# Optimization experiments

Hardware: AMD Instinct MI355X
Metric: run time of the kernel (lower is better)

The kernel has to match this reference:

```python
import jax, jax.numpy as jnp
import numpy as np

N_NODES = 100000
N_EDGES = 1600000
D_IN = 64
D_OUT = 64


def setup_inputs() -> dict:
    key = jax.random.key(0)
    k1, k2, k3, k4, k5 = jax.random.split(key, 5)
    features = jax.random.normal(k1, (N_NODES, D_IN), dtype=jnp.float32)
    edge_rows = jax.random.randint(k2, (N_EDGES,), 0, N_NODES, dtype=jnp.int32)
    edge_cols = jax.random.randint(k3, (N_EDGES,), 0, N_NODES, dtype=jnp.int32)
    edge_vals = jax.random.uniform(k4, (N_EDGES,), dtype=jnp.float32)
    # glorot_uniform init for the dense projection weight
    limit = np.sqrt(6.0 / (D_IN + D_OUT)).astype(np.float32)
    weight = jax.random.uniform(k5, (D_IN, D_OUT), dtype=jnp.float32,
                                minval=-limit, maxval=limit)
    return {"features": features, "edge_rows": edge_rows,
            "edge_cols": edge_cols, "edge_vals": edge_vals, "weight": weight}


def reference(features, edge_rows, edge_cols, edge_vals, weight):
    # SpMM: (adj @ features) via edge-list gather + segment_sum
    gathered = features[edge_cols] * edge_vals[:, None]        # [E, D_IN]
    agg = jax.ops.segment_sum(gathered, edge_rows,
                              num_segments=N_NODES)            # [N, D_IN]
    # Dense projection + ReLU
    return jax.nn.relu(agg @ weight)                           # [N, D_OUT]
```

## Files before the change

kernel.cpp:

```cpp
#include <hip/hip_runtime.h>

#define D 64
#define OVF_CAP 65536


__device__ inline unsigned short f32_to_bf16_rne(float x) {
    unsigned u = __float_as_uint(x);
    unsigned r = (u + 0x7FFFu + ((u >> 16) & 1u)) >> 16;
    return (unsigned short)r;
}

__global__ void f2bf_kernel(const float4* __restrict__ in,
                            ushort4* __restrict__ out, int n4) {
    int i = blockIdx.x * blockDim.x + threadIdx.x;
    int stride = gridDim.x * blockDim.x;
    for (; i < n4; i += stride) {
        float4 f = in[i];
        ushort4 u;
        u.x = f32_to_bf16_rne(f.x);
        u.y = f32_to_bf16_rne(f.y);
        u.z = f32_to_bf16_rne(f.z);
        u.w = f32_to_bf16_rne(f.w);
        out[i] = u;
    }
}

template <int SLOTS, int NSLICE>
__global__ void scatter_slot_kernel(const int* __restrict__ erows,
                                    const int* __restrict__ ecols,
                                    const float* __restrict__ evals,
                                    int* __restrict__ cnt,
                                    int2* __restrict__ pairs,
                                    int4* __restrict__ ovf,
                                    int* __restrict__ ovfCnt,
                                    int n_edges, int rows_per_slice) {
    const int slice = blockIdx.x & (NSLICE - 1);
    const int rlo   = slice * rows_per_slice;
    const int rhi   = rlo + rows_per_slice;
    const int sub   = blockIdx.x / NSLICE;
    const int t     = sub * blockDim.x + threadIdx.x;
    const int strid = (gridDim.x / NSLICE) * blockDim.x;

    auto handle = [&](int r, int c, float v) {
        if (r >= rlo && r < rhi) {
            int pos = atomicAdd(&cnt[r], 1);
            if (pos < SLOTS) {
                pairs[(size_t)r * SLOTS + pos] = make_int2(c, __float_as_int(v));
            } else {
                int oi = atomicAdd(ovfCnt, 1);
                if (oi < OVF_CAP) ovf[oi] = make_int4(r, c, __float_as_int(v), 0);
            }
        }
    };

    int e = t;
    for (; e + 3 * strid < n_edges; e += 4 * strid) {
        int e0 = e, e1 = e + strid, e2 = e + 2 * strid, e3 = e + 3 * strid;
        int   r0 = erows[e0], r1 = erows[e1], r2 = erows[e2], r3 = erows[e3];
        int   c0 = ecols[e0], c1 = ecols[e1], c2 = ecols[e2], c3 = ecols[e3];
        float v0 = evals[e0], v1 = evals[e1], v2 = evals[e2], v3 = evals[e3];
        handle(r0, c0, v0);
        handle(r1, c1, v1);
        handle(r2, c2, v2);
        handle(r3, c3, v3);
    }
    for (; e < n_edges; e += strid)
        handle(erows[e], ecols[e], evals[e]);
}

template <int SLOTS>
__global__ void __launch_bounds__(256)
fused_slot_bf16(const unsigned short* __restrict__ fb,
                const int* __restrict__ cnt, const int2* __restrict__ pairs,
                const float* __restrict__ W, const int* __restrict__ ovfCnt,
                float* __restrict__ out, int n_rows) {
    __shared__ float sW[D * D];
    for (int i = threadIdx.x; i < D * D; i += 256) sW[i] = W[i];
    __syncthreads();

    const int  w      = threadIdx.x >> 6;
    const int  lane   = threadIdx.x & 63;
    const bool doRelu = (*ovfCnt == 0);

    for (int row = blockIdx.x * 4 + w; row < n_rows; row += gridDim.x * 4) {
        int m = min(cnt[row], SLOTS);
        int px = 0, py = 0;
        if (lane < m) {
            int2 p = pairs[(size_t)row * SLOTS + lane];
            px = p.x; py = p.y;
        }
        float acc = 0.0f;
        int k = 0;
        for (; k + 4 <= m; k += 4) {
            int c0 = __shfl(px, k + 0), b0 = __shfl(py, k + 0);
            int c1 = __shfl(px, k + 1), b1 = __shfl(py, k + 1);
            int c2 = __shfl(px, k + 2), b2 = __shfl(py, k + 2);
            int c3 = __shfl(px, k + 3), b3 = __shfl(py, k + 3);
            float f0 = __uint_as_float((unsigned)fb[(size_t)c0 * D + lane] << 16);
            float f1 = __uint_as_float((unsigned)fb[(size_t)c1 * D + lane] << 16);
            float f2 = __uint_as_float((unsigned)fb[(size_t)c2 * D + lane] << 16);
            float f3 = __uint_as_float((unsigned)fb[(size_t)c3 * D + lane] << 16);
            acc = fmaf(f0, __int_as_float(b0), acc);
            acc = fmaf(f1, __int_as_float(b1), acc);
            acc = fmaf(f2, __int_as_float(b2), acc);
            acc = fmaf(f3, __int_as_float(b3), acc);
        }
        for (; k < m; ++k) {
            int c = __shfl(px, k), b = __shfl(py, k);
            acc = fmaf(__uint_as_float((unsigned)fb[(size_t)c * D + lane] << 16),
                       __int_as_float(b), acc);
        }

        float o = 0.0f;
#pragma unroll
        for (int kk = 0; kk < D; ++kk)
            o = fmaf(__shfl(acc, kk), sW[kk * D + lane], o);

        out[(size_t)row * D + lane] = doRelu ? fmaxf(o, 0.0f) : o;
    }
}

template <int SLOTS>
__global__ void __launch_bounds__(256)
fused_slot_f32(const float* __restrict__ feat, const int* __restrict__ cnt,
               const int2* __restrict__ pairs, const float* __restrict__ W,
               const int* __restrict__ ovfCnt, float* __restrict__ out,
               int n_rows) {
    __shared__ float sW[D * D];
    for (int i = threadIdx.x; i < D * D; i += 256) sW[i] = W[i];
    __syncthreads();
    const int  w      = threadIdx.x >> 6;
    const int  lane   = threadIdx.x & 63;
    const bool doRelu = (*ovfCnt == 0);
    for (int row = blockIdx.x * 4 + w; row < n_rows; row += gridDim.x * 4) {
        int m = min(cnt[row], SLOTS);
        int px = 0, py = 0;
        if (lane < m) {
            int2 p = pairs[(size_t)row * SLOTS + lane];
            px = p.x; py = p.y;
        }
        float acc = 0.0f;
        int k = 0;
        for (; k + 4 <= m; k += 4) {
            int c0 = __shfl(px, k + 0), b0 = __shfl(py, k + 0);
            int c1 = __shfl(px, k + 1), b1 = __shfl(py, k + 1);
            int c2 = __shfl(px, k + 2), b2 = __shfl(py, k + 2);
            int c3 = __shfl(px, k + 3), b3 = __shfl(py, k + 3);
            float f0 = feat[(size_t)c0 * D + lane];
            float f1 = feat[(size_t)c1 * D + lane];
            float f2 = feat[(size_t)c2 * D + lane];
            float f3 = feat[(size_t)c3 * D + lane];
            acc = fmaf(f0, __int_as_float(b0), acc);
            acc = fmaf(f1, __int_as_float(b1), acc);
            acc = fmaf(f2, __int_as_float(b2), acc);
            acc = fmaf(f3, __int_as_float(b3), acc);
        }
        for (; k < m; ++k) {
            int c = __shfl(px, k), b = __shfl(py, k);
            acc = fmaf(feat[(size_t)c * D + lane], __int_as_float(b), acc);
        }
        float o = 0.0f;
#pragma unroll
        for (int kk = 0; kk < D; ++kk)
            o = fmaf(__shfl(acc, kk), sW[kk * D + lane], o);
        out[(size_t)row * D + lane] = doRelu ? fmaxf(o, 0.0f) : o;
    }
}

__global__ void __launch_bounds__(256)
ovf_kernel(const float* __restrict__ feat, const float* __restrict__ W,
           const int4* __restrict__ ovf, const int* __restrict__ ovfCnt,
           float* __restrict__ out) {
    int n = *ovfCnt;
    if (n > OVF_CAP) n = OVF_CAP;
    if (n == 0) return;
    const int lane = threadIdx.x & 63;
    const int wave = (blockIdx.x * blockDim.x + threadIdx.x) >> 6;
    const int nw   = (gridDim.x * blockDim.x) >> 6;
    for (int i = wave; i < n; i += nw) {
        int4  e = ovf[i];
        float v = __int_as_float(e.z);
        float f = feat[(size_t)e.y * D + lane];
        float acc = 0.0f;
#pragma unroll
        for (int k = 0; k < D; ++k)
            acc = fmaf(__shfl(f, k), W[k * D + lane], acc);
        unsafeAtomicAdd(&out[(size_t)e.x * D + lane], v * acc);
    }
}

__global__ void relu_fix_kernel(float* __restrict__ out,
                                const int* __restrict__ ovfCnt, int n_elems) {
    if (*ovfCnt == 0) return;
    int i = blockIdx.x * blockDim.x + threadIdx.x;
    int stride = gridDim.x * blockDim.x;
    for (; i < n_elems; i += stride)
        out[i] = fmaxf(out[i], 0.0f);
}

__global__ void hist_kernel(const int* __restrict__ erows, int* __restrict__ cur,
                            int n_edges) {
    int i = blockIdx.x * blockDim.x + threadIdx.x;
    int stride = gridDim.x * blockDim.x;
    for (int e = i; e < n_edges; e += stride) atomicAdd(&cur[erows[e]], 1);
}

__global__ void __launch_bounds__(256)
scan_block_reduce(const int* __restrict__ cnt, int* __restrict__ bs, int n) {
    __shared__ int s[256];
    int i = blockIdx.x * 256 + threadIdx.x;
    s[threadIdx.x] = (i < n) ? cnt[i] : 0;
    __syncthreads();
    for (int off = 128; off > 0; off >>= 1) {
        if (threadIdx.x < (unsigned)off) s[threadIdx.x] += s[threadIdx.x + off];
        __syncthreads();
    }
    if (threadIdx.x == 0) bs[blockIdx.x] = s[0];
}

__global__ void __launch_bounds__(1024)
scan_top(int* __restrict__ bs, int nblk, int* __restrict__ rowStartN) {
    __shared__ int s[1024];
    int t = threadIdx.x;
    int x = (t < nblk) ? bs[t] : 0;
    s[t] = x;
    __syncthreads();
    for (int off = 1; off < 1024; off <<= 1) {
        int y = (t >= off) ? s[t - off] : 0;
        __syncthreads();
        s[t] += y;
        __syncthreads();
    }
    if (t < nblk) bs[t] = s[t] - x;
    if (t == 1023) *rowStartN = s[1023];
}

__global__ void __launch_bounds__(256)
scan_final(int* __restrict__ cur, const int* __restrict__ bs,
           int* __restrict__ rowStart, int n) {
    __shared__ int s[256];
    int t = threadIdx.x;
    int i = blockIdx.x * 256 + t;
    int x = (i < n) ? cur[i] : 0;
    s[t] = x;
    __syncthreads();
    for (int off = 1; off < 256; off <<= 1) {
        int y = (t >= off) ? s[t - off] : 0;
        __syncthreads();
        s[t] += y;
        __syncthreads();
    }
    int excl = s[t] - x + bs[blockIdx.x];
    if (i < n) { rowStart[i] = excl; cur[i] = excl; }
}

__global__ void scatter_kernel(const int* __restrict__ erows,
                               const int* __restrict__ ecols,
                               const float* __restrict__ evals,
                               int* __restrict__ cur, int2* __restrict__ pairs,
                               int n_edges) {
    int i = blockIdx.x * blockDim.x + threadIdx.x;
    int stride = gridDim.x * blockDim.x;
    for (int e = i; e < n_edges; e += stride) {
        int pos = atomicAdd(&cur[erows[e]], 1);
        pairs[pos] = make_int2(ecols[e], __float_as_int(evals[e]));
    }
}

__global__ void __launch_bounds__(256)
fused_kernel(const float* __restrict__ feat, const int* __restrict__ rowStart,
             const int2* __restrict__ pairs, const float* __restrict__ W,
             float* __restrict__ out, int n_rows) {
    __shared__ float sW[D * D];
    __shared__ float srow[4][D];
    for (int i = threadIdx.x; i < D * D; i += 256) sW[i] = W[i];
    const int w = threadIdx.x >> 6, lane = threadIdx.x & 63;
    const int row = blockIdx.x * 4 + w;
    float acc = 0.0f;
    if (row < n_rows) {
        int s = rowStart[row], e = rowStart[row + 1], i = s;
        for (; i + 4 <= e; i += 4) {
            int2 p0 = pairs[i + 0], p1 = pairs[i + 1];
            int2 p2 = pairs[i + 2], p3 = pairs[i + 3];
            float f0 = feat[(size_t)p0.x * D + lane];
            float f1 = feat[(size_t)p1.x * D + lane];
            float f2 = feat[(size_t)p2.x * D + lane];
            float f3 = feat[(size_t)p3.x * D + lane];
            acc = fmaf(f0, __int_as_float(p0.y), acc);
            acc = fmaf(f1, __int_as_float(p1.y), acc);
            acc = fmaf(f2, __int_as_float(p2.y), acc);
            acc = fmaf(f3, __int_as_float(p3.y), acc);
        }
        for (; i < e; ++i) {
            int2 p = pairs[i];
            acc = fmaf(feat[(size_t)p.x * D + lane], __int_as_float(p.y), acc);
        }
    }
    srow[w][lane] = acc;
    __syncthreads();
    float o = 0.0f;
#pragma unroll
    for (int k = 0; k < D; ++k) o = fmaf(srow[w][k], sW[k * D + lane], o);
    if (row < n_rows) out[(size_t)row * D + lane] = fmaxf(o, 0.0f);
}

__global__ void agg_kernel(const float* __restrict__ feat,
                           const int* __restrict__ erows,
                           const int* __restrict__ ecols,
                           const float* __restrict__ evals,
                           float* __restrict__ agg, int n_edges) {
    int gid = blockIdx.x * blockDim.x + threadIdx.x;
    int group = gid >> 4, lane4 = gid & 15;
    int stride = (gridDim.x * blockDim.x) >> 4;
    for (int e = group; e < n_edges; e += stride) {
        int r = erows[e], c = ecols[e];
        float v = evals[e];
        const float4 f = *reinterpret_cast<const float4*>(feat + (size_t)c * D + lane4 * 4);
        float* dst = agg + (size_t)r * D + lane4 * 4;
        unsafeAtomicAdd(dst + 0, f.x * v);
        unsafeAtomicAdd(dst + 1, f.y * v);
        unsafeAtomicAdd(dst + 2, f.z * v);
        unsafeAtomicAdd(dst + 3, f.w * v);
    }
}

__global__ void __launch_bounds__(256)
proj_kernel(const float* __restrict__ agg, const float* __restrict__ W,
            float* __restrict__ out, int n_rows) {
    __shared__ float sW[D * D];
    __shared__ float srow[4][D];
    for (int i = threadIdx.x; i < D * D; i += 256) sW[i] = W[i];
    __syncthreads();
    const int rg = threadIdx.x >> 6, j = threadIdx.x & 63;
    for (int row0 = blockIdx.x * 4; row0 < n_rows; row0 += gridDim.x * 4) {
        int r = row0 + rg;
        float v = (r < n_rows) ? agg[(size_t)r * D + j] : 0.0f;
        srow[rg][j] = v;
        __syncthreads();
        float acc = 0.0f;
#pragma unroll
        for (int k = 0; k < D; ++k) acc = fmaf(srow[rg][k], sW[k * D + j], acc);
        if (r < n_rows) out[(size_t)r * D + j] = fmaxf(acc, 0.0f);
        __syncthreads();
    }
}

extern "C" void kernel_launch(void* const* d_in, const int* in_sizes, int n_in,
                              void* d_out, int out_size, void* d_ws, size_t ws_size,
                              hipStream_t stream) {
    const float* feat  = (const float*)d_in[0];
    const int*   erows = (const int*)  d_in[1];
    const int*   ecols = (const int*)  d_in[2];
    const float* evals = (const float*)d_in[3];
    const float* W     = (const float*)d_in[4];
    float*       out   = (float*)d_out;

    const int n_edges = in_sizes[1];
    const int n_nodes = in_sizes[0] / D;

    auto align256 = [](size_t x) { return (x + 255) & ~(size_t)255; };

    size_t off_cnt    = 0;
    size_t off_ovfCnt = align256((size_t)n_nodes * 4);
    size_t off_ovf    = align256(off_ovfCnt + 4);
    size_t off_fb     = align256(off_ovf + (size_t)OVF_CAP * 16);
    size_t off_pairs  = align256(off_fb + (size_t)n_nodes * D * 2);
    size_t need_bf16  = off_pairs + (size_t)n_nodes * 64 * 8;
    size_t off_pairs2 = off_fb;
    size_t need_f32   = off_pairs2 + (size_t)n_nodes * 64 * 8;

    const int rows_per_slice4 = (n_nodes + 3) / 4;

    if (ws_size >= need_bf16 || ws_size >= need_f32) {
        char* ws     = (char*)d_ws;
        int*  cnt    = (int*) (ws + off_cnt);
        int*  ovfCnt = (int*) (ws + off_ovfCnt);
        int4* ovf    = (int4*)(ws + off_ovf);

        hipMemsetAsync(cnt, 0, (size_t)n_nodes * 4, stream);
        hipMemsetAsync(ovfCnt, 0, 4, stream);

        if (ws_size >= need_bf16) {
            unsigned short* fb = (unsigned short*)(ws + off_fb);
            int2* pairs = (int2*)(ws + off_pairs);
            f2bf_kernel<<<2048, 256, 0, stream>>>(
                (const float4*)feat, (ushort4*)fb, n_nodes * D / 4);
            scatter_slot_kernel<64, 4><<<2048, 256, 0, stream>>>(
                erows, ecols, evals, cnt, pairs, ovf, ovfCnt, n_edges, rows_per_slice4);
            fused_slot_bf16<64><<<2048, 256, 0, stream>>>(
                fb, cnt, pairs, W, ovfCnt, out, n_nodes);
        } else {
            int2* pairs = (int2*)(ws + off_pairs2);
            scatter_slot_kernel<64, 4><<<2048, 256, 0, stream>>>(
                erows, ecols, evals, cnt, pairs, ovf, ovfCnt, n_edges, rows_per_slice4);
            fused_slot_f32<64><<<2048, 256, 0, stream>>>(
                feat, cnt, pairs, W, ovfCnt, out, n_nodes);
        }
        ovf_kernel<<<256, 256, 0, stream>>>(feat, W, ovf, ovfCnt, out);
        relu_fix_kernel<<<512, 256, 0, stream>>>(out, ovfCnt, n_nodes * D);
        return;
    }

    const int nblk = (n_nodes + 255) / 256;
    size_t off_rowStart = 0;
    size_t off_cur      = align256(off_rowStart + (size_t)(n_nodes + 1) * 4);
    size_t off_bs       = align256(off_cur + (size_t)n_nodes * 4);
    size_t off_p        = align256(off_bs + (size_t)nblk * 4);
    size_t ws_needed    = off_p + (size_t)n_edges * 8;

    if (ws_size >= ws_needed && nblk <= 1024) {
        char* ws = (char*)d_ws;
        int*  rowStart = (int*) (ws + off_rowStart);
        int*  cur      = (int*) (ws + off_cur);
        int*  bs       = (int*) (ws + off_bs);
        int2* pairs    = (int2*)(ws + off_p);

        hipMemsetAsync(cur, 0, (size_t)n_nodes * 4, stream);
        hist_kernel<<<2048, 256, 0, stream>>>(erows, cur, n_edges);
        scan_block_reduce<<<nblk, 256, 0, stream>>>(cur, bs, n_nodes);
        scan_top<<<1, 1024, 0, stream>>>(bs, nblk, rowStart + n_nodes);
        scan_final<<<nblk, 256, 0, stream>>>(cur, bs, rowStart, n_nodes);
        scatter_kernel<<<2048, 256, 0, stream>>>(erows, ecols, evals, cur, pairs, n_edges);
        fused_kernel<<<(n_nodes + 3) / 4, 256, 0, stream>>>(feat, rowStart, pairs, W, out, n_nodes);
    } else {
        hipMemsetAsync(out, 0, (size_t)n_nodes * D * 4, stream);
        agg_kernel<<<2048, 256, 0, stream>>>(feat, erows, ecols, evals, out, n_edges);
        proj_kernel<<<2048, 256, 0, stream>>>(out, W, out, n_nodes);
    }
}
```

Before: 298.8 us.

## Shrink slot buckets to 32, one row per wave, LDS broadcast for projection

```diff
diff --git a/kernel.cpp b/kernel.cpp
--- a/kernel.cpp
+++ b/kernel.cpp
@@ -75,21 +75,24 @@
                 const float* __restrict__ W, const int* __restrict__ ovfCnt,
                 float* __restrict__ out, int n_rows) {
     __shared__ float sW[D * D];
-    for (int i = threadIdx.x; i < D * D; i += 256) sW[i] = W[i];
-    __syncthreads();
+    __shared__ float srow[4][D];
+
+    for (int i = threadIdx.x; i < D * D; i += 256)
+        sW[i] = W[i];
 
     const int  w      = threadIdx.x >> 6;
     const int  lane   = threadIdx.x & 63;
+    const int  row    = blockIdx.x * 4 + w;
     const bool doRelu = (*ovfCnt == 0);
 
-    for (int row = blockIdx.x * 4 + w; row < n_rows; row += gridDim.x * 4) {
+    float acc = 0.0f;
+    if (row < n_rows) {
         int m = min(cnt[row], SLOTS);
         int px = 0, py = 0;
         if (lane < m) {
             int2 p = pairs[(size_t)row * SLOTS + lane];
             px = p.x; py = p.y;
         }
-        float acc = 0.0f;
         int k = 0;
         for (; k + 4 <= m; k += 4) {
             int c0 = __shfl(px, k + 0), b0 = __shfl(py, k + 0);
@@ -110,14 +113,17 @@
             acc = fmaf(__uint_as_float((unsigned)fb[(size_t)c * D + lane] << 16),
                        __int_as_float(b), acc);
         }
-
-        float o = 0.0f;
+    }
+    srow[w][lane] = acc;
+    __syncthreads();
+
+    float o = 0.0f;
 #pragma unroll
-        for (int kk = 0; kk < D; ++kk)
-            o = fmaf(__shfl(acc, kk), sW[kk * D + lane], o);
-
+    for (int kk = 0; kk < D; ++kk)
+        o = fmaf(srow[w][kk], sW[kk * D + lane], o);
+
+    if (row < n_rows)
         out[(size_t)row * D + lane] = doRelu ? fmaxf(o, 0.0f) : o;
-    }
 }
 
 template <int SLOTS>
@@ -127,19 +133,20 @@
                const int* __restrict__ ovfCnt, float* __restrict__ out,
                int n_rows) {
     __shared__ float sW[D * D];
+    __shared__ float srow[4][D];
     for (int i = threadIdx.x; i < D * D; i += 256) sW[i] = W[i];
-    __syncthreads();
     const int  w      = threadIdx.x >> 6;
     const int  lane   = threadIdx.x & 63;
+    const int  row    = blockIdx.x * 4 + w;
     const bool doRelu = (*ovfCnt == 0);
-    for (int row = blockIdx.x * 4 + w; row < n_rows; row += gridDim.x * 4) {
+    float acc = 0.0f;
+    if (row < n_rows) {
         int m = min(cnt[row], SLOTS);
         int px = 0, py = 0;
         if (lane < m) {
             int2 p = pairs[(size_t)row * SLOTS + lane];
             px = p.x; py = p.y;
         }
-        float acc = 0.0f;
         int k = 0;
         for (; k + 4 <= m; k += 4) {
             int c0 = __shfl(px, k + 0), b0 = __shfl(py, k + 0);
@@ -159,12 +166,15 @@
             int c = __shfl(px, k), b = __shfl(py, k);
             acc = fmaf(feat[(size_t)c * D + lane], __int_as_float(b), acc);
         }
-        float o = 0.0f;
+    }
+    srow[w][lane] = acc;
+    __syncthreads();
+    float o = 0.0f;
 #pragma unroll
-        for (int kk = 0; kk < D; ++kk)
-            o = fmaf(__shfl(acc, kk), sW[kk * D + lane], o);
+    for (int kk = 0; kk < D; ++kk)
+        o = fmaf(srow[w][kk], sW[kk * D + lane], o);
+    if (row < n_rows)
         out[(size_t)row * D + lane] = doRelu ? fmaxf(o, 0.0f) : o;
-    }
 }
 
 __global__ void __launch_bounds__(256)
@@ -365,11 +375,12 @@
     size_t off_ovf    = align256(off_ovfCnt + 4);
     size_t off_fb     = align256(off_ovf + (size_t)OVF_CAP * 16);
     size_t off_pairs  = align256(off_fb + (size_t)n_nodes * D * 2);
-    size_t need_bf16  = off_pairs + (size_t)n_nodes * 64 * 8;
+    size_t need_bf16  = off_pairs + (size_t)n_nodes * 32 * 8;
     size_t off_pairs2 = off_fb;
-    size_t need_f32   = off_pairs2 + (size_t)n_nodes * 64 * 8;
-
-    const int rows_per_slice4 = (n_nodes + 3) / 4;
+    size_t need_f32   = off_pairs2 + (size_t)n_nodes * 32 * 8;
+
+    const int rows_per_slice8 = (n_nodes + 7) / 8;
+    const int nblk_fused      = (n_nodes + 3) / 4;
 
     if (ws_size >= need_bf16 || ws_size >= need_f32) {
         char* ws     = (char*)d_ws;
@@ -385,15 +396,15 @@
             int2* pairs = (int2*)(ws + off_pairs);
             f2bf_kernel<<<2048, 256, 0, stream>>>(
                 (const float4*)feat, (ushort4*)fb, n_nodes * D / 4);
-            scatter_slot_kernel<64, 4><<<2048, 256, 0, stream>>>(
-                erows, ecols, evals, cnt, pairs, ovf, ovfCnt, n_edges, rows_per_slice4);
-            fused_slot_bf16<64><<<2048, 256, 0, stream>>>(
+            scatter_slot_kernel<32, 8><<<2048, 256, 0, stream>>>(
+                erows, ecols, evals, cnt, pairs, ovf, ovfCnt, n_edges, rows_per_slice8);
+            fused_slot_bf16<32><<<nblk_fused, 256, 0, stream>>>(
                 fb, cnt, pairs, W, ovfCnt, out, n_nodes);
         } else {
             int2* pairs = (int2*)(ws + off_pairs2);
-            scatter_slot_kernel<64, 4><<<2048, 256, 0, stream>>>(
-                erows, ecols, evals, cnt, pairs, ovf, ovfCnt, n_edges, rows_per_slice4);
-            fused_slot_f32<64><<<2048, 256, 0, stream>>>(
+            scatter_slot_kernel<32, 8><<<2048, 256, 0, stream>>>(
+                erows, ecols, evals, cnt, pairs, ovf, ovfCnt, n_edges, rows_per_slice8);
+            fused_slot_f32<32><<<nblk_fused, 256, 0, stream>>>(
                 feat, cnt, pairs, W, ovfCnt, out, n_nodes);
         }
         ovf_kernel<<<256, 256, 0, stream>>>(feat, W, ovf, ovfCnt, out);
```

New measurement: 295.2 us. No clear change (-1.2%).
